# Kernel tuning notes

Hardware: AMD Instinct MI355X
Metric: run time of the kernel (lower is better)

The kernel has to match this reference:

```python
import jax, jax.numpy as jnp
import numpy as np

N, E = 50000, 800000
IN_CH, H, OUT_CH, ED, L = 64, 128, 128, 1, 4


def setup_inputs() -> dict:
    key = jax.random.key(0)
    ks = jax.random.split(key, 24)
    s = 0.02
    inp = {
        'h': jax.random.normal(ks[0], (N, IN_CH), jnp.float32),
        'coords': jax.random.normal(ks[1], (N, 3), jnp.float32),
        'edge_attr': jax.random.normal(ks[2], (E, ED), jnp.float32),
        'emb_in_W': jax.random.normal(ks[3], (IN_CH, H), jnp.float32) * s,
        'emb_in_b': jnp.zeros((H,), jnp.float32),
        'emb_out_W': jax.random.normal(ks[4], (H, OUT_CH), jnp.float32) * s,
        'emb_out_b': jnp.zeros((OUT_CH,), jnp.float32),
        # per-layer stacked params
        'eW1': jax.random.normal(ks[5], (L, 2 * H + 1 + ED, H), jnp.float32) * s,
        'eb1': jnp.zeros((L, H), jnp.float32),
        'eW2': jax.random.normal(ks[6], (L, H, H), jnp.float32) * s,
        'eb2': jnp.zeros((L, H), jnp.float32),
        'cW1': jax.random.normal(ks[7], (L, H, H), jnp.float32) * s,
        'cb1': jnp.zeros((L, H), jnp.float32),
        'cWc': jax.random.normal(ks[8], (L, H, 1), jnp.float32) * 0.001,  # xavier gain=0.001, no bias
        'nW1': jax.random.normal(ks[9], (L, 2 * H, H), jnp.float32) * s,
        'nb1': jnp.zeros((L, H), jnp.float32),
        'nW2': jax.random.normal(ks[10], (L, H, H), jnp.float32) * s,
        'nb2': jnp.zeros((L, H), jnp.float32),
        'edge_index': jax.random.randint(ks[11], (2, E), 0, N, jnp.int32),
    }
    return inp


def _egnn_forward(h, coords, edge_attr, emb_in_W, emb_in_b, emb_out_W, emb_out_b,
                  eW1, eb1, eW2, eb2, cW1, cb1, cWc, nW1, nb1, nW2, nb2, edge_index):
    silu = jax.nn.silu
    row, col = edge_index[0], edge_index[1]  # PyG: j=source=row, i=target=col
    # count of incoming edges per target node, for coords_agg='mean'
    counts = jax.ops.segment_sum(jnp.ones((E,), jnp.float32), col, num_segments=N)
    counts = jnp.maximum(counts, 1.0)[:, None]
    h = h @ emb_in_W + emb_in_b
    for l in range(L):
        coord_diff = coords[row] - coords[col]                       # [E,3]
        dist = jnp.sum(coord_diff * coord_diff, axis=-1, keepdims=True)  # [E,1]
        # message: edge MLP on cat(x_i, x_j, dist, edge_attr)
        edge_in = jnp.concatenate([h[col], h[row], dist, edge_attr], axis=-1)
        ef = silu(edge_in @ eW1[l] + eb1[l])
        ef = silu(ef @ eW2[l] + eb2[l])                               # [E,H]
        cw = silu(ef @ cW1[l] + cb1[l]) @ cWc[l]                      # [E,1]
        coord_upd = coord_diff * cw                                   # [E,3]
        # aggregate to target nodes
        agg_feat = jax.ops.segment_sum(ef, col, num_segments=N)       # [N,H]
        agg_coord = jax.ops.segment_sum(coord_upd, col, num_segments=N) / counts
        # node update (residual)
        node_in = jnp.concatenate([h, agg_feat], axis=-1)
        upd = silu(node_in @ nW1[l] + nb1[l]) @ nW2[l] + nb2[l]
        h = h + upd
        coords = coords + agg_coord
    h = h @ emb_out_W + emb_out_b
    return h, coords


def reference(h, coords, edge_attr, emb_in_W, emb_in_b, emb_out_W, emb_out_b,
              eW1, eb1, eW2, eb2, cW1, cb1, cWc, nW1, nb1, nW2, nb2, edge_index):
    return _egnn_forward(h, coords, edge_attr, emb_in_W, emb_in_b, emb_out_W, emb_out_b,
                         eW1, eb1, eW2, eb2, cW1, cb1, cWc, nW1, nb1, nW2, nb2, edge_index)
```

## Files before the change

kernel.cpp:

```cpp
#include <hip/hip_runtime.h>

constexpr int Nn = 50000;
constexpr int Ee = 800000;
constexpr int EIN_STR = 296;
constexpr int EF_STR  = 136;
constexpr int NIN_STR = 264;
constexpr int HIN_STR = 72;

typedef short s8v __attribute__((ext_vector_type(8)));
typedef float f4v __attribute__((ext_vector_type(4)));

__device__ __forceinline__ ushort f2bf(float f) {
    uint u = __float_as_uint(f);
    uint r = (u + 0x7FFFu + ((u >> 16) & 1u)) >> 16;
    return (ushort)r;
}
__device__ __forceinline__ float bf2f(ushort s) {
    return __uint_as_float(((uint)s) << 16);
}
__device__ __forceinline__ float silu_f(float x) {
    return x * __fdividef(1.0f, 1.0f + __expf(-x));
}

__global__ void __launch_bounds__(256) k_swzg(
    const float* __restrict__ src, ushort* __restrict__ dst, int K, int KC, int total)
{
    int gid = blockIdx.x * 256 + threadIdx.x;
    if (gid >= total) return;
    int per = KC * 4096;
    int l = gid / per, r = gid % per;
    int fb = r >> 9, rem = r & 511;
    int lane = rem >> 3, jj = rem & 7;
    int kc = fb >> 3, t = fb & 7;
    int k = kc * 32 + ((lane >> 4) << 3) + jj;
    int n = t * 16 + (lane & 15);
    float v = (k < K) ? src[(size_t)l * K * 128 + (size_t)k * 128 + n] : 0.0f;
    dst[gid] = f2bf(v);
}

__global__ void __launch_bounds__(256) k_count(const int* __restrict__ eidx, int* __restrict__ ecnt)
{
    int e = blockIdx.x * 256 + threadIdx.x;
    atomicAdd(&ecnt[eidx[Ee + e]], 1);
}

__global__ void __launch_bounds__(1024) k_scan(const int* __restrict__ ecnt, int* __restrict__ cursor)
{
    __shared__ int wsum[16];
    __shared__ int carry;
    int tid = threadIdx.x, lane = tid & 63, w = tid >> 6;
    if (tid == 0) carry = 0;
    __syncthreads();
    for (int start = 0; start < Nn; start += 1024) {
        int i = start + tid;
        int x = (i < Nn) ? ecnt[i] : 0;
        int c0 = carry;
        int s = x;
        #pragma unroll
        for (int off = 1; off < 64; off <<= 1) {
            int t = __shfl_up(s, off, 64);
            if (lane >= off) s += t;
        }
        if (lane == 63) wsum[w] = s;
        __syncthreads();
        if (w == 0) {
            int t = (lane < 16) ? wsum[lane] : 0;
            #pragma unroll
            for (int off = 1; off < 16; off <<= 1) {
                int u = __shfl_up(t, off, 64);
                if (lane >= off) t += u;
            }
            if (lane < 16) wsum[lane] = t;
        }
        __syncthreads();
        int woff = (w == 0) ? 0 : wsum[w - 1];
        if (i < Nn) cursor[i] = c0 + woff + s - x;
        int blocksum = wsum[15];
        __syncthreads();
        if (tid == 0) carry = c0 + blocksum;
        __syncthreads();
    }
}

__global__ void __launch_bounds__(256) k_scatter(
    const int* __restrict__ eidx, const float* __restrict__ edge_attr,
    int* __restrict__ cursor,
    int* __restrict__ srow, int* __restrict__ scol, float* __restrict__ sattr)
{
    int e = blockIdx.x * 256 + threadIdx.x;
    int r = eidx[e], c = eidx[Ee + e];
    int p = atomicAdd(&cursor[c], 1);
    srow[p] = r; scol[p] = c; sattr[p] = edge_attr[e];
}

__global__ void __launch_bounds__(512, 2) k_emb(
    const float* __restrict__ h_in, const float* __restrict__ coords,
    const ushort* __restrict__ ws_, const float* __restrict__ b,
    float* __restrict__ hbuf, ushort* __restrict__ hbf, float* __restrict__ cbuf)
{
    __shared__ alignas(16) ushort s_h[64 * HIN_STR];
    const int tid = threadIdx.x;
    const int nb = blockIdx.x * 64;
    #pragma unroll
    for (int i = 0; i < 2; i++) {
        int idx = i * 512 + tid;
        int e = idx >> 4, ch = idx & 15;
        int node = nb + e;
        float4 f = make_float4(0.f, 0.f, 0.f, 0.f);
        if (node < Nn) f = *(const float4*)(h_in + (size_t)node * 64 + ch * 4);
        ushort4 u; u.x = f2bf(f.x); u.y = f2bf(f.y); u.z = f2bf(f.z); u.w = f2bf(f.w);
        *(ushort4*)(s_h + e * HIN_STR + ch * 4) = u;
    }
    if (tid < 192) {
        int n = nb + tid / 3, d = tid % 3;
        if (n < Nn) cbuf[n * 3 + d] = coords[n * 3 + d];
    }
    __syncthreads();
    const int lane = tid & 63, wave = tid >> 6;
    const int m = lane & 15, quad = lane >> 4;
    const int ws2 = wave >> 2, wt = wave & 3;
    f4v acc[2][2];
    #pragma unroll
    for (int mt = 0; mt < 2; mt++) { acc[mt][0] = (f4v){0,0,0,0}; acc[mt][1] = (f4v){0,0,0,0}; }
    const ushort* bBase = ws_ + wt * 1024 + lane * 8;
    #pragma unroll
    for (int kc = 0; kc < 2; kc++) {
        s8v b0 = *(const s8v*)(bBase + kc * 4096);
        s8v b1v = *(const s8v*)(bBase + kc * 4096 + 512);
        #pragma unroll
        for (int mt = 0; mt < 2; mt++) {
            s8v a = *(const s8v*)(s_h + (ws2 * 32 + mt * 16 + m) * HIN_STR + kc * 32 + quad * 8);
            acc[mt][0] = __builtin_amdgcn_mfma_f32_16x16x32_bf16(a, b0, acc[mt][0], 0, 0, 0);
            acc[mt][1] = __builtin_amdgcn_mfma_f32_16x16x32_bf16(a, b1v, acc[mt][1], 0, 0, 0);
        }
    }
    #pragma unroll
    for (int tt = 0; tt < 2; tt++) {
        int col = (wt * 2 + tt) * 16 + m;
        float bias = b[col];
        #pragma unroll
        for (int mt = 0; mt < 2; mt++)
            #pragma unroll
            for (int r = 0; r < 4; r++) {
                int node = nb + ws2 * 32 + mt * 16 + quad * 4 + r;
                if (node < Nn) {
                    float v = acc[mt][tt][r] + bias;
                    hbuf[(size_t)node * 128 + col] = v;
                    hbf[(size_t)node * 128 + col] = f2bf(v);
                }
            }
    }
}

__global__ void __launch_bounds__(512, 2) k_edge(
    const ushort* __restrict__ hbf, const float* __restrict__ cbuf,
    const int* __restrict__ srow, const int* __restrict__ scol, const float* __restrict__ sattr,
    const ushort* __restrict__ w1s, const float* __restrict__ b1,
    const ushort* __restrict__ w2s, const float* __restrict__ b2,
    const ushort* __restrict__ cw1s, const float* __restrict__ cb1,
    const float* __restrict__ cwc,
    float* __restrict__ agg_feat, float* __restrict__ agg_coord)
{
    __shared__ alignas(16) ushort s_ein[64 * EIN_STR];
    __shared__ alignas(16) ushort s_efa[64 * EF_STR];
    __shared__ alignas(16) ushort s_efb[64 * EF_STR];
    __shared__ int   s_col[64];
    __shared__ int   s_row[64];
    __shared__ float s_cd[64 * 3];
    __shared__ float s_cw[64];

    const int tid = threadIdx.x;
    const int eb = blockIdx.x * 64;

    if (tid < 64) {
        int rw = srow[eb + tid], cl = scol[eb + tid];
        s_row[tid] = rw; s_col[tid] = cl;
        float d0 = cbuf[rw * 3 + 0] - cbuf[cl * 3 + 0];
        float d1 = cbuf[rw * 3 + 1] - cbuf[cl * 3 + 1];
        float d2 = cbuf[rw * 3 + 2] - cbuf[cl * 3 + 2];
        s_cd[tid * 3 + 0] = d0; s_cd[tid * 3 + 1] = d1; s_cd[tid * 3 + 2] = d2;
        float dist = d0 * d0 + d1 * d1 + d2 * d2;
        s_ein[tid * EIN_STR + 256] = f2bf(dist);
        s_ein[tid * EIN_STR + 257] = f2bf(sattr[eb + tid]);
        uint* zp = (uint*)(s_ein + tid * EIN_STR + 258);
        #pragma unroll
        for (int z = 0; z < 15; z++) zp[z] = 0;
        s_cw[tid] = 0.0f;
    }
    __syncthreads();

    #pragma unroll
    for (int i = 0; i < 4; i++) {
        int idx = i * 512 + tid;
        int e = idx >> 5, ch = idx & 31;
        int node = (ch < 16) ? s_col[e] : s_row[e];
        uint4 v = *(const uint4*)(hbf + (size_t)node * 128 + (ch & 15) * 8);
        *(uint4*)(s_ein + e * EIN_STR + ch * 8) = v;
    }
    __syncthreads();

    const int lane = tid & 63, wave = tid >> 6;
    const int m = lane & 15, quad = lane >> 4;
    const int ws2 = wave >> 2, wt = wave & 3;
    const int rbase = ws2 * 32;

    {
        f4v acc[2][2];
        #pragma unroll
        for (int mt = 0; mt < 2; mt++) { acc[mt][0] = (f4v){0,0,0,0}; acc[mt][1] = (f4v){0,0,0,0}; }
        const ushort* bBase = w1s + wt * 1024 + (size_t)lane * 8;
        #pragma unroll
        for (int kc = 0; kc < 9; kc++) {
            s8v b0 = *(const s8v*)(bBase + kc * 4096);
            s8v b1v = *(const s8v*)(bBase + kc * 4096 + 512);
            #pragma unroll
            for (int mt = 0; mt < 2; mt++) {
                s8v a = *(const s8v*)(s_ein + (rbase + mt * 16 + m) * EIN_STR + kc * 32 + quad * 8);
                acc[mt][0] = __builtin_amdgcn_mfma_f32_16x16x32_bf16(a, b0, acc[mt][0], 0, 0, 0);
                acc[mt][1] = __builtin_amdgcn_mfma_f32_16x16x32_bf16(a, b1v, acc[mt][1], 0, 0, 0);
            }
        }
        #pragma unroll
        for (int tt = 0; tt < 2; tt++) {
            int col = (wt * 2 + tt) * 16 + m;
            float bias = b1[col];
            #pragma unroll
            for (int mt = 0; mt < 2; mt++)
                #pragma unroll
                for (int r = 0; r < 4; r++)
                    s_efa[(rbase + mt * 16 + quad * 4 + r) * EF_STR + col] = f2bf(silu_f(acc[mt][tt][r] + bias));
        }
    }
    __syncthreads();

    {
        f4v acc[2][2];
        #pragma unroll
        for (int mt = 0; mt < 2; mt++) { acc[mt][0] = (f4v){0,0,0,0}; acc[mt][1] = (f4v){0,0,0,0}; }
        const ushort* bBase = w2s + wt * 1024 + (size_t)lane * 8;
        #pragma unroll
        for (int kc = 0; kc < 4; kc++) {
            s8v b0 = *(const s8v*)(bBase + kc * 4096);
            s8v b1v = *(const s8v*)(bBase + kc * 4096 + 512);
            #pragma unroll
            for (int mt = 0; mt < 2; mt++) {
                s8v a = *(const s8v*)(s_efa + (rbase + mt * 16 + m) * EF_STR + kc * 32 + quad * 8);
                acc[mt][0] = __builtin_amdgcn_mfma_f32_16x16x32_bf16(a, b0, acc[mt][0], 0, 0, 0);
                acc[mt][1] = __builtin_amdgcn_mfma_f32_16x16x32_bf16(a, b1v, acc[mt][1], 0, 0, 0);
            }
        }
        #pragma unroll
        for (int tt = 0; tt < 2; tt++) {
            int col = (wt * 2 + tt) * 16 + m;
            float bias = b2[col];
            #pragma unroll
            for (int mt = 0; mt < 2; mt++)
                #pragma unroll
                for (int r = 0; r < 4; r++)
                    s_efb[(rbase + mt * 16 + quad * 4 + r) * EF_STR + col] = f2bf(silu_f(acc[mt][tt][r] + bias));
        }
    }
    __syncthreads();

    {
        f4v acc[2][2];
        #pragma unroll
        for (int mt = 0; mt < 2; mt++) { acc[mt][0] = (f4v){0,0,0,0}; acc[mt][1] = (f4v){0,0,0,0}; }
        const ushort* bBase = cw1s + wt * 1024 + (size_t)lane * 8;
        #pragma unroll
        for (int kc = 0; kc < 4; kc++) {
            s8v b0 = *(const s8v*)(bBase + kc * 4096);
            s8v b1v = *(const s8v*)(bBase + kc * 4096 + 512);
            #pragma unroll
            for (int mt = 0; mt < 2; mt++) {
                s8v a = *(const s8v*)(s_efb + (rbase + mt * 16 + m) * EF_STR + kc * 32 + quad * 8);
                acc[mt][0] = __builtin_amdgcn_mfma_f32_16x16x32_bf16(a, b0, acc[mt][0], 0, 0, 0);
                acc[mt][1] = __builtin_amdgcn_mfma_f32_16x16x32_bf16(a, b1v, acc[mt][1], 0, 0, 0);
            }
        }
        int c0 = wt * 32 + m, c1 = wt * 32 + 16 + m;
        float bias0 = cb1[c0], wc0 = cwc[c0];
        float bias1 = cb1[c1], wc1 = cwc[c1];
        #pragma unroll
        for (int mt = 0; mt < 2; mt++) {
            float p0 = silu_f(acc[mt][0][0] + bias0) * wc0 + silu_f(acc[mt][1][0] + bias1) * wc1;
            float p1 = silu_f(acc[mt][0][1] + bias0) * wc0 + silu_f(acc[mt][1][1] + bias1) * wc1;
            float p2 = silu_f(acc[mt][0][2] + bias0) * wc0 + silu_f(acc[mt][1][2] + bias1) * wc1;
            float p3 = silu_f(acc[mt][0][3] + bias0) * wc0 + silu_f(acc[mt][1][3] + bias1) * wc1;
            #pragma unroll
            for (int off = 1; off < 16; off <<= 1) {
                p0 += __shfl_xor(p0, off, 64);
                p1 += __shfl_xor(p1, off, 64);
                p2 += __shfl_xor(p2, off, 64);
                p3 += __shfl_xor(p3, off, 64);
            }
            if (m < 4) {
                float v = (m == 0) ? p0 : (m == 1) ? p1 : (m == 2) ? p2 : p3;
                atomicAdd(&s_cw[rbase + mt * 16 + quad * 4 + m], v);
            }
        }
    }
    __syncthreads();

    if (tid < 12) {
        int d = tid % 3, seg = tid / 3;
        int e0 = seg * 16;
        float acc = 0.0f; int cur = s_col[e0];
        for (int e = e0; e < e0 + 16; e++) {
            int c = s_col[e];
            if (c != cur) {
                unsafeAtomicAdd(&agg_coord[cur * 3 + d], acc);
                acc = 0.0f; cur = c;
            }
            acc += s_cd[e * 3 + d] * s_cw[e];
        }
        unsafeAtomicAdd(&agg_coord[cur * 3 + d], acc);
    }

    {
        int j = tid & 127;
        int e0 = (tid >> 7) * 16;
        float acc = 0.0f; int cur = s_col[e0];
        #pragma unroll 4
        for (int e = e0; e < e0 + 16; e++) {
            int c = s_col[e];
            if (c != cur) {
                unsafeAtomicAdd(&agg_feat[(size_t)cur * 128 + j], acc);
                acc = 0.0f; cur = c;
            }
            acc += bf2f(s_efb[e * EF_STR + j]);
        }
        unsafeAtomicAdd(&agg_feat[(size_t)cur * 128 + j], acc);
    }
}

__global__ void __launch_bounds__(512, 2) k_node(
    float* __restrict__ hbuf, ushort* __restrict__ hbf, float* __restrict__ cbuf,
    const float* __restrict__ agg_feat, const float* __restrict__ agg_coord,
    const int* __restrict__ ecnt,
    const ushort* __restrict__ w1s, const float* __restrict__ b1,
    const ushort* __restrict__ w2s, const float* __restrict__ b2)
{
    __shared__ alignas(16) ushort s_nin[64 * NIN_STR];
    __shared__ alignas(16) ushort s_t1[64 * EF_STR];
    const int tid = threadIdx.x;
    const int nb = blockIdx.x * 64;

    #pragma unroll
    for (int i = 0; i < 2; i++) {
        int idx = i * 512 + tid;
        int e = idx >> 4, ch = idx & 15;
        int node = nb + e;
        uint4 v = make_uint4(0, 0, 0, 0);
        if (node < Nn) v = *(const uint4*)(hbf + (size_t)node * 128 + ch * 8);
        *(uint4*)(s_nin + e * NIN_STR + ch * 8) = v;
    }
    #pragma unroll
    for (int i = 0; i < 4; i++) {
        int idx = i * 512 + tid;
        int e = idx >> 5, ch = idx & 31;
        int node = nb + e;
        float4 f = make_float4(0.f, 0.f, 0.f, 0.f);
        if (node < Nn) f = *(const float4*)(agg_feat + (size_t)node * 128 + ch * 4);
        ushort4 u; u.x = f2bf(f.x); u.y = f2bf(f.y); u.z = f2bf(f.z); u.w = f2bf(f.w);
        *(ushort4*)(s_nin + e * NIN_STR + 128 + ch * 4) = u;
    }
    if (tid < 64) {
        int n = nb + tid;
        if (n < Nn) {
            float c = (float)ecnt[n]; c = (c < 1.0f) ? 1.0f : c;
            float inv = __fdividef(1.0f, c);
            cbuf[n * 3 + 0] += agg_coord[n * 3 + 0] * inv;
            cbuf[n * 3 + 1] += agg_coord[n * 3 + 1] * inv;
            cbuf[n * 3 + 2] += agg_coord[n * 3 + 2] * inv;
        }
    }
    __syncthreads();

    const int lane = tid & 63, wave = tid >> 6;
    const int m = lane & 15, quad = lane >> 4;
    const int ws2 = wave >> 2, wt = wave & 3;
    const int rbase = ws2 * 32;

    {
        f4v acc[2][2];
        #pragma unroll
        for (int mt = 0; mt < 2; mt++) { acc[mt][0] = (f4v){0,0,0,0}; acc[mt][1] = (f4v){0,0,0,0}; }
        const ushort* bBase = w1s + wt * 1024 + (size_t)lane * 8;
        #pragma unroll
        for (int kc = 0; kc < 8; kc++) {
            s8v b0 = *(const s8v*)(bBase + kc * 4096);
            s8v b1v = *(const s8v*)(bBase + kc * 4096 + 512);
            #pragma unroll
            for (int mt = 0; mt < 2; mt++) {
                s8v a = *(const s8v*)(s_nin + (rbase + mt * 16 + m) * NIN_STR + kc * 32 + quad * 8);
                acc[mt][0] = __builtin_amdgcn_mfma_f32_16x16x32_bf16(a, b0, acc[mt][0], 0, 0, 0);
                acc[mt][1] = __builtin_amdgcn_mfma_f32_16x16x32_bf16(a, b1v, acc[mt][1], 0, 0, 0);
            }
        }
        #pragma unroll
        for (int tt = 0; tt < 2; tt++) {
            int col = (wt * 2 + tt) * 16 + m;
            float bias = b1[col];
            #pragma unroll
            for (int mt = 0; mt < 2; mt++)
                #pragma unroll
                for (int r = 0; r < 4; r++)
                    s_t1[(rbase + mt * 16 + quad * 4 + r) * EF_STR + col] = f2bf(silu_f(acc[mt][tt][r] + bias));
        }
    }
    __syncthreads();

    {
        f4v acc[2][2];
        #pragma unroll
        for (int mt = 0; mt < 2; mt++) { acc[mt][0] = (f4v){0,0,0,0}; acc[mt][1] = (f4v){0,0,0,0}; }
        const ushort* bBase = w2s + wt * 1024 + (size_t)lane * 8;
        #pragma unroll
        for (int kc = 0; kc < 4; kc++) {
            s8v b0 = *(const s8v*)(bBase + kc * 4096);
            s8v b1v = *(const s8v*)(bBase + kc * 4096 + 512);
            #pragma unroll
            for (int mt = 0; mt < 2; mt++) {
                s8v a = *(const s8v*)(s_t1 + (rbase + mt * 16 + m) * EF_STR + kc * 32 + quad * 8);
                acc[mt][0] = __builtin_amdgcn_mfma_f32_16x16x32_bf16(a, b0, acc[mt][0], 0, 0, 0);
                acc[mt][1] = __builtin_amdgcn_mfma_f32_16x16x32_bf16(a, b1v, acc[mt][1], 0, 0, 0);
            }
        }
        #pragma unroll
        for (int tt = 0; tt < 2; tt++) {
            int col = (wt * 2 + tt) * 16 + m;
            float bias = b2[col];
            #pragma unroll
            for (int mt = 0; mt < 2; mt++)
                #pragma unroll
                for (int r = 0; r < 4; r++) {
                    int node = nb + rbase + mt * 16 + quad * 4 + r;
                    if (node < Nn) {
                        float v = hbuf[(size_t)node * 128 + col] + acc[mt][tt][r] + bias;
                        hbuf[(size_t)node * 128 + col] = v;
                        hbf[(size_t)node * 128 + col] = f2bf(v);
                    }
                }
        }
    }
}

__global__ void __launch_bounds__(512, 2) k_emb_out(
    const ushort* __restrict__ hbf, const float* __restrict__ cbuf,
    const ushort* __restrict__ ws_, const float* __restrict__ b, float* __restrict__ out)
{
    __shared__ alignas(16) ushort s_h[64 * EF_STR];
    const int tid = threadIdx.x;
    const int nb = blockIdx.x * 64;
    #pragma unroll
    for (int i = 0; i < 2; i++) {
        int idx = i * 512 + tid;
        int e = idx >> 4, ch = idx & 15;
        int node = nb + e;
        uint4 v = make_uint4(0, 0, 0, 0);
        if (node < Nn) v = *(const uint4*)(hbf + (size_t)node * 128 + ch * 8);
        *(uint4*)(s_h + e * EF_STR + ch * 8) = v;
    }
    if (tid < 192) {
        int n = nb + tid / 3, d = tid % 3;
        if (n < Nn) out[(size_t)Nn * 128 + n * 3 + d] = cbuf[n * 3 + d];
    }
    __syncthreads();
    const int lane = tid & 63, wave = tid >> 6;
    const int m = lane & 15, quad = lane >> 4;
    const int ws2 = wave >> 2, wt = wave & 3;
    f4v acc[2][2];
    #pragma unroll
    for (int mt = 0; mt < 2; mt++) { acc[mt][0] = (f4v){0,0,0,0}; acc[mt][1] = (f4v){0,0,0,0}; }
    const ushort* bBase = ws_ + wt * 1024 + (size_t)lane * 8;
    #pragma unroll
    for (int kc = 0; kc < 4; kc++) {
        s8v b0 = *(const s8v*)(bBase + kc * 4096);
        s8v b1v = *(const s8v*)(bBase + kc * 4096 + 512);
        #pragma unroll
        for (int mt = 0; mt < 2; mt++) {
            s8v a = *(const s8v*)(s_h + (ws2 * 32 + mt * 16 + m) * EF_STR + kc * 32 + quad * 8);
            acc[mt][0] = __builtin_amdgcn_mfma_f32_16x16x32_bf16(a, b0, acc[mt][0], 0, 0, 0);
            acc[mt][1] = __builtin_amdgcn_mfma_f32_16x16x32_bf16(a, b1v, acc[mt][1], 0, 0, 0);
        }
    }
    #pragma unroll
    for (int tt = 0; tt < 2; tt++) {
        int col = (wt * 2 + tt) * 16 + m;
        float bias = b[col];
        #pragma unroll
        for (int mt = 0; mt < 2; mt++)
            #pragma unroll
            for (int r = 0; r < 4; r++) {
                int node = nb + ws2 * 32 + mt * 16 + quad * 4 + r;
                if (node < Nn) out[(size_t)node * 128 + col] = acc[mt][tt][r] + bias;
            }
    }
}

extern "C" void kernel_launch(void* const* d_in, const int* in_sizes, int n_in,
                              void* d_out, int out_size, void* d_ws, size_t ws_size,
                              hipStream_t stream)
{
    const float* h_in      = (const float*)d_in[0];
    const float* coords    = (const float*)d_in[1];
    const float* edge_attr = (const float*)d_in[2];
    const float* emb_in_W  = (const float*)d_in[3];
    const float* emb_in_b  = (const float*)d_in[4];
    const float* emb_out_W = (const float*)d_in[5];
    const float* emb_out_b = (const float*)d_in[6];
    const float* eW1 = (const float*)d_in[7];
    const float* eb1 = (const float*)d_in[8];
    const float* eW2 = (const float*)d_in[9];
    const float* eb2 = (const float*)d_in[10];
    const float* cW1 = (const float*)d_in[11];
    const float* cb1 = (const float*)d_in[12];
    const float* cWc = (const float*)d_in[13];
    const float* nW1 = (const float*)d_in[14];
    const float* nb1 = (const float*)d_in[15];
    const float* nW2 = (const float*)d_in[16];
    const float* nb2 = (const float*)d_in[17];
    const int*  eidx = (const int*)d_in[18];

    size_t off = 0;
    char* base = (char*)d_ws;
    auto alloc = [&](size_t bytes) -> char* {
        char* p = base + off;
        off += (bytes + 255) & ~(size_t)255;
        return p;
    };
    float*  hbuf      = (float*)alloc((size_t)Nn * 128 * 4);
    ushort* hbf       = (ushort*)alloc((size_t)Nn * 128 * 2);
    float*  cbuf      = (float*)alloc((size_t)Nn * 3 * 4);
    int*    ecnt      = (int*)alloc((size_t)Nn * 4);
    int*    cursor    = (int*)alloc((size_t)Nn * 4);
    int*    srow      = (int*)alloc((size_t)Ee * 4);
    int*    scol      = (int*)alloc((size_t)Ee * 4);
    float*  sattr     = (float*)alloc((size_t)Ee * 4);
    float*  agg_feat  = (float*)alloc((size_t)Nn * 128 * 4);
    float*  agg_coord = (float*)alloc((size_t)Nn * 3 * 4);
    ushort* eW1s      = (ushort*)alloc((size_t)4 * 36864 * 2);
    ushort* eW2s      = (ushort*)alloc((size_t)4 * 16384 * 2);
    ushort* cW1s      = (ushort*)alloc((size_t)4 * 16384 * 2);
    ushort* nW1s      = (ushort*)alloc((size_t)4 * 32768 * 2);
    ushort* nW2s      = (ushort*)alloc((size_t)4 * 16384 * 2);
    ushort* eInWs     = (ushort*)alloc((size_t)8192 * 2);
    ushort* eOutWs    = (ushort*)alloc((size_t)16384 * 2);

    k_swzg<<<(4*9*4096+255)/256, 256, 0, stream>>>(eW1, eW1s, 258, 9, 4*9*4096);
    k_swzg<<<(4*4*4096+255)/256, 256, 0, stream>>>(eW2, eW2s, 128, 4, 4*4*4096);
    k_swzg<<<(4*4*4096+255)/256, 256, 0, stream>>>(cW1, cW1s, 128, 4, 4*4*4096);
    k_swzg<<<(4*8*4096+255)/256, 256, 0, stream>>>(nW1, nW1s, 256, 8, 4*8*4096);
    k_swzg<<<(4*4*4096+255)/256, 256, 0, stream>>>(nW2, nW2s, 128, 4, 4*4*4096);
    k_swzg<<<(2*4096+255)/256,   256, 0, stream>>>(emb_in_W,  eInWs,  64, 2, 2*4096);
    k_swzg<<<(4*4096+255)/256,   256, 0, stream>>>(emb_out_W, eOutWs, 128, 4, 4*4096);

    hipMemsetAsync(ecnt, 0, (size_t)Nn * 4, stream);
    k_count<<<Ee / 256, 256, 0, stream>>>(eidx, ecnt);
    k_scan<<<1, 1024, 0, stream>>>(ecnt, cursor);
    k_scatter<<<Ee / 256, 256, 0, stream>>>(eidx, edge_attr, cursor, srow, scol, sattr);
    k_emb<<<(Nn + 63) / 64, 512, 0, stream>>>(h_in, coords, eInWs, emb_in_b, hbuf, hbf, cbuf);

    for (int l = 0; l < 4; l++) {
        hipMemsetAsync(agg_feat, 0, (size_t)Nn * 128 * 4, stream);
        hipMemsetAsync(agg_coord, 0, (size_t)Nn * 3 * 4, stream);
        k_edge<<<Ee / 64, 512, 0, stream>>>(
            hbf, cbuf, srow, scol, sattr,
            eW1s + (size_t)l * 36864, eb1 + l * 128,
            eW2s + (size_t)l * 16384, eb2 + l * 128,
            cW1s + (size_t)l * 16384, cb1 + l * 128,
            cWc + l * 128,
            agg_feat, agg_coord);
        k_node<<<(Nn + 63) / 64, 512, 0, stream>>>(
            hbuf, hbf, cbuf, agg_feat, agg_coord, ecnt,
            nW1s + (size_t)l * 32768, nb1 + l * 128,
            nW2s + (size_t)l * 16384, nb2 + l * 128);
    }
    k_emb_out<<<(Nn + 63) / 64, 512, 0, stream>>>(hbf, cbuf, eOutWs, emb_out_b, (float*)d_out);
}
```

Baseline: 1.753 ms.

## Shrink edge-kernel shared memory and raise occupancy with buffer reuse

Shrinks the edge kernel's LDS footprint from three large tiles to two reused 64x136 buffers plus a small tail tile for dist/attr, and raises launch bounds from 2 to 6 blocks per CU. The aim is more concurrent blocks to hide gather and atomic latency. Also removes a sync before the gather, replaces the LDS-atomic coord-weight reduction with shuffles into per-slot partials, and switches bf16 conversion to truncation. The tighter launch bound may force register spills, and truncation changes numerics slightly.

```diff
diff --git a/kernel.cpp b/kernel.cpp
--- a/kernel.cpp
+++ b/kernel.cpp
@@ -2,8 +2,8 @@
 
 constexpr int Nn = 50000;
 constexpr int Ee = 800000;
-constexpr int EIN_STR = 296;
 constexpr int EF_STR  = 136;
+constexpr int TL_STR  = 40;
 constexpr int NIN_STR = 264;
 constexpr int HIN_STR = 72;
 
@@ -14,6 +14,9 @@
     uint u = __float_as_uint(f);
     uint r = (u + 0x7FFFu + ((u >> 16) & 1u)) >> 16;
     return (ushort)r;
+}
+__device__ __forceinline__ ushort f2bf_t(float f) {
+    return (ushort)(__float_as_uint(f) >> 16);
 }
 __device__ __forceinline__ float bf2f(ushort s) {
     return __uint_as_float(((uint)s) << 16);
@@ -152,7 +155,7 @@
     }
 }
 
-__global__ void __launch_bounds__(512, 2) k_edge(
+__global__ void __launch_bounds__(512, 6) k_edge(
     const ushort* __restrict__ hbf, const float* __restrict__ cbuf,
     const int* __restrict__ srow, const int* __restrict__ scol, const float* __restrict__ sattr,
     const ushort* __restrict__ w1s, const float* __restrict__ b1,
@@ -161,41 +164,38 @@
     const float* __restrict__ cwc,
     float* __restrict__ agg_feat, float* __restrict__ agg_coord)
 {
-    __shared__ alignas(16) ushort s_ein[64 * EIN_STR];
-    __shared__ alignas(16) ushort s_efa[64 * EF_STR];
-    __shared__ alignas(16) ushort s_efb[64 * EF_STR];
+    __shared__ alignas(16) ushort s_a[64 * EF_STR];
+    __shared__ alignas(16) ushort s_b[64 * EF_STR];
+    __shared__ alignas(16) ushort s_t[64 * TL_STR];
     __shared__ int   s_col[64];
-    __shared__ int   s_row[64];
     __shared__ float s_cd[64 * 3];
-    __shared__ float s_cw[64];
 
     const int tid = threadIdx.x;
     const int eb = blockIdx.x * 64;
 
     if (tid < 64) {
         int rw = srow[eb + tid], cl = scol[eb + tid];
-        s_row[tid] = rw; s_col[tid] = cl;
+        s_col[tid] = cl;
         float d0 = cbuf[rw * 3 + 0] - cbuf[cl * 3 + 0];
         float d1 = cbuf[rw * 3 + 1] - cbuf[cl * 3 + 1];
         float d2 = cbuf[rw * 3 + 2] - cbuf[cl * 3 + 2];
         s_cd[tid * 3 + 0] = d0; s_cd[tid * 3 + 1] = d1; s_cd[tid * 3 + 2] = d2;
         float dist = d0 * d0 + d1 * d1 + d2 * d2;
-        s_ein[tid * EIN_STR + 256] = f2bf(dist);
-        s_ein[tid * EIN_STR + 257] = f2bf(sattr[eb + tid]);
-        uint* zp = (uint*)(s_ein + tid * EIN_STR + 258);
+        s_t[tid * TL_STR + 0] = f2bf(dist);
+        s_t[tid * TL_STR + 1] = f2bf(sattr[eb + tid]);
+        uint* zp = (uint*)(s_t + tid * TL_STR + 2);
         #pragma unroll
         for (int z = 0; z < 15; z++) zp[z] = 0;
-        s_cw[tid] = 0.0f;
-    }
-    __syncthreads();
-
+    }
     #pragma unroll
     for (int i = 0; i < 4; i++) {
         int idx = i * 512 + tid;
         int e = idx >> 5, ch = idx & 31;
-        int node = (ch < 16) ? s_col[e] : s_row[e];
+        int node = (ch < 16) ? scol[eb + e] : srow[eb + e];
         uint4 v = *(const uint4*)(hbf + (size_t)node * 128 + (ch & 15) * 8);
-        *(uint4*)(s_ein + e * EIN_STR + ch * 8) = v;
+        ushort* dst = (ch < 16) ? (s_a + e * EF_STR + ch * 8)
+                                : (s_b + e * EF_STR + (ch - 16) * 8);
+        *(uint4*)dst = v;
     }
     __syncthreads();
 
@@ -204,137 +204,341 @@
     const int ws2 = wave >> 2, wt = wave & 3;
     const int rbase = ws2 * 32;
 
-    {
-        f4v acc[2][2];
-        #pragma unroll
-        for (int mt = 0; mt < 2; mt++) { acc[mt][0] = (f4v){0,0,0,0}; acc[mt][1] = (f4v){0,0,0,0}; }
+    f4v acc[2][2];
+    #pragma unroll
+    for (int mt = 0; mt < 2; mt++) { acc[mt][0] = (f4v){0,0,0,0}; acc[mt][1] = (f4v){0,0,0,0}; }
+    {
         const ushort* bBase = w1s + wt * 1024 + (size_t)lane * 8;
         #pragma unroll
-        for (int kc = 0; kc < 9; kc++) {
-            s8v b0 = *(const s8v*)(bBase + kc * 4096);
-            s8v b1v = *(const s8v*)(bBase + kc * 4096 + 512);
-            #pragma unroll
-            for (int mt = 0; mt < 2; mt++) {
-                s8v a = *(const s8v*)(s_ein + (rbase + mt * 16 + m) * EIN_STR + kc * 32 + quad * 8);
+        for (int kc = 0; kc < 4; kc++) {
+            s8v b0 = *(const s8v*)(bBase + kc * 4096);
+            s8v b1v = *(const s8v*)(bBase + kc * 4096 + 512);
+            #pragma unroll
+            for (int mt = 0; mt < 2; mt++) {
+                s8v a = *(const s8v*)(s_a + (rbase + mt * 16 + m) * EF_STR + kc * 32 + quad * 8);
                 acc[mt][0] = __builtin_amdgcn_mfma_f32_16x16x32_bf16(a, b0, acc[mt][0], 0, 0, 0);
                 acc[mt][1] = __builtin_amdgcn_mfma_f32_16x16x32_bf16(a, b1v, acc[mt][1], 0, 0, 0);
             }
         }
         #pragma unroll
+        for (int kc = 4; kc < 8; kc++) {
+            s8v b0 = *(const s8v*)(bBase + kc * 4096);
+            s8v b1v = *(const s8v*)(bBase + kc * 4096 + 512);
+            #pragma unroll
+            for (int mt = 0; mt < 2; mt++) {
+                s8v a = *(const s8v*)(s_b + (rbase + mt * 16 + m) * EF_STR + (kc - 4) * 32 + quad * 8);
+                acc[mt][0] = __builtin_amdgcn_mfma_f32_16x16x32_bf16(a, b0, acc[mt][0], 0, 0, 0);
+                acc[mt][1] = __builtin_amdgcn_mfma_f32_16x16x32_bf16(a, b1v, acc[mt][1], 0, 0, 0);
+            }
+        }
+        {
+            s8v b0 = *(const s8v*)(bBase + 8 * 4096);
+            s8v b1v = *(const s8v*)(bBase + 8 * 4096 + 512);
+            #pragma unroll
+            for (int mt = 0; mt < 2; mt++) {
+                s8v a = *(const s8v*)(s_t + (rbase + mt * 16 + m) * TL_STR + quad * 8);
+                acc[mt][0] = __builtin_amdgcn_mfma_f32_16x16x32_bf16(a, b0, acc[mt][0], 0, 0, 0);
+                acc[mt][1] = __builtin_amdgcn_mfma_f32_16x16x32_bf16(a, b1v, acc[mt][1], 0, 0, 0);
+            }
+        }
+    }
+    __syncthreads();
+
+    #pragma unroll
+    for (int tt = 0; tt < 2; tt++) {
+        int col = (wt * 2 + tt) * 16 + m;
+        float bias = b1[col];
+        #pragma unroll
+        for (int mt = 0; mt < 2; mt++)
+            #pragma unroll
+            for (int r = 0; r < 4; r++)
+                s_a[(rbase + mt * 16 + quad * 4 + r) * EF_STR + col] = f2bf_t(silu_f(acc[mt][tt][r] + bias));
+    }
+    __syncthreads();
+
+    {
+        f4v acc2[2][2];
+        #pragma unroll
+        for (int mt = 0; mt < 2; mt++) { acc2[mt][0] = (f4v){0,0,0,0}; acc2[mt][1] = (f4v){0,0,0,0}; }
+        const ushort* bBase = w2s + wt * 1024 + (size_t)lane * 8;
+        #pragma unroll
+        for (int kc = 0; kc < 4; kc++) {
+            s8v b0 = *(const s8v*)(bBase + kc * 4096);
+            s8v b1v = *(const s8v*)(bBase + kc * 4096 + 512);
+            #pragma unroll
+            for (int mt = 0; mt < 2; mt++) {
+                s8v a = *(const s8v*)(s_a + (rbase + mt * 16 + m) * EF_STR + kc * 32 + quad * 8);
+                acc2[mt][0] = __builtin_amdgcn_mfma_f32_16x16x32_bf16(a, b0, acc2[mt][0], 0, 0, 0);
+                acc2[mt][1] = __builtin_amdgcn_mfma_f32_16x16x32_bf16(a, b1v, acc2[mt][1], 0, 0, 0);
+            }
+        }
+        #pragma unroll
         for (int tt = 0; tt < 2; tt++) {
             int col = (wt * 2 + tt) * 16 + m;
-            float bias = b1[col];
+            float bias = b2[col];
             #pragma unroll
             for (int mt = 0; mt < 2; mt++)
                 #pragma unroll
                 for (int r = 0; r < 4; r++)
-                    s_efa[(rbase + mt * 16 + quad * 4 + r) * EF_STR + col] = f2bf(silu_f(acc[mt][tt][r] + bias));
-        }
-    }
-    __syncthreads();
-
-    {
-        f4v acc[2][2];
-        #pragma unroll
-        for (int mt = 0; mt < 2; mt++) { acc[mt][0] = (f4v){0,0,0,0}; acc[mt][1] = (f4v){0,0,0,0}; }
-        const ushort* bBase = w2s + wt * 1024 + (size_t)lane * 8;
+                    s_b[(rbase + mt * 16 + quad * 4 + r) * EF_STR + col] = f2bf_t(silu_f(acc2[mt][tt][r] + bias));
+        }
+    }
+    __syncthreads();
+
+    {
+        f4v acc3[2][2];
+        #pragma unroll
+        for (int mt = 0; mt < 2; mt++) { acc3[mt][0] = (f4v){0,0,0,0}; acc3[mt][1] = (f4v){0,0,0,0}; }
+        const ushort* bBase = cw1s + wt * 1024 + (size_t)lane * 8;
         #pragma unroll
         for (int kc = 0; kc < 4; kc++) {
             s8v b0 = *(const s8v*)(bBase + kc * 4096);
             s8v b1v = *(const s8v*)(bBase + kc * 4096 + 512);
             #pragma unroll
             for (int mt = 0; mt < 2; mt++) {
-                s8v a = *(const s8v*)(s_efa + (rbase + mt * 16 + m) * EF_STR + kc * 32 + quad * 8);
-                acc[mt][0] = __builtin_amdgcn_mfma_f32_16x16x32_bf16(a, b0, acc[mt][0], 0, 0, 0);
-                acc[mt][1] = __builtin_amdgcn_mfma_f32_16x16x32_bf16(a, b1v, acc[mt][1], 0, 0, 0);
-            }
-        }
-        #pragma unroll
-        for (int tt = 0; tt < 2; tt++) {
-            int col = (wt * 2 + tt) * 16 + m;
-            float bias = b2[col];
-            #pragma unroll
-            for (int mt = 0; mt < 2; mt++)
-                #pragma unroll
-                for (int r = 0; r < 4; r++)
-                    s_efb[(rbase + mt * 16 + quad * 4 + r) * EF_STR + col] = f2bf(silu_f(acc[mt][tt][r] + bias));
-        }
-    }
-    __syncthreads();
-
-    {
-        f4v acc[2][2];
-        #pragma unroll
-        for (int mt = 0; mt < 2; mt++) { acc[mt][0] = (f4v){0,0,0,0}; acc[mt][1] = (f4v){0,0,0,0}; }
-        const ushort* bBase = cw1s + wt * 1024 + (size_t)lane * 8;
-        #pragma unroll
-        for (int kc = 0; kc < 4; kc++) {
-            s8v b0 = *(const s8v*)(bBase + kc * 4096);
-            s8v b1v = *(const s8v*)(bBase + kc * 4096 + 512);
-            #pragma unroll
-            for (int mt = 0; mt < 2; mt++) {
-                s8v a = *(const s8v*)(s_efb + (rbase + mt * 16 + m) * EF_STR + kc * 32 + quad * 8);
-                acc[mt][0] = __builtin_amdgcn_mfma_f32_16x16x32_bf16(a, b0, acc[mt][0], 0, 0, 0);
-                acc[mt][1] = __builtin_amdgcn_mfma_f32_16x16x32_bf16(a, b1v, acc[mt][1], 0, 0, 0);
+                s8v a = *(const s8v*)(s_b + (rbase + mt * 16 + m) * EF_STR + kc * 32 + quad * 8);
+                acc3[mt][0] = __builtin_amdgcn_mfma_f32_16x16x32_bf16(a, b0, acc3[mt][0], 0, 0, 0);
+                acc3[mt][1] = __builtin_amdgcn_mfma_f32_16x16x32_bf16(a, b1v, acc3[mt][1], 0, 0, 0);
             }
         }
         int c0 = wt * 32 + m, c1 = wt * 32 + 16 + m;
         float bias0 = cb1[c0], wc0 = cwc[c0];
         float bias1 = cb1[c1], wc1 = cwc[c1];
-        #pragma unroll
-        for (int mt = 0; mt < 2; mt++) {
-            float p0 = silu_f(acc[mt][0][0] + bias0) * wc0 + silu_f(acc[mt][1][0] + bias1) * wc1;
-            float p1 = silu_f(acc[mt][0][1] + bias0) * wc0 + silu_f(acc[mt][1][1] + bias1) * wc1;
-            float p2 = silu_f(acc[mt][0][2] + bias0) * wc0 + silu_f(acc[mt][1][2] + bias1) * wc1;
-            float p3 = silu_f(acc[mt][0][3] + bias0) * wc0 + silu_f(acc[mt][1][3] + bias1) * wc1;
-            #pragma unroll
-            for (int off = 1; off < 16; off <<= 1) {
-                p0 += __shfl_xor(p0, off, 64);
-                p1 += __shfl_xor(p1, off, 64);
-                p2 += __shfl_xor(p2, off, 64);
-                p3 += __shfl_xor(p3, off, 64);
-            }
-            if (m < 4) {
-                float v = (m == 0) ? p0 : (m == 1) ? p1 : (m == 2) ? p2 : p3;
-                atomicAdd(&s_cw[rbase + mt * 16 + quad * 4 + m], v);
-            }
-        }
-    }
-    __syncthreads();
-
-    if (tid < 12) {
-        int d = tid % 3, seg = tid / 3;
-        int e0 = seg * 16;
-        float acc = 0.0f; int cur = s_col[e0];
-        for (int e = e0; e < e0 + 16; e++) {
-            int c = s_col[e];
-            if (c != cur) {
-                unsafeAtomicAdd(&agg_coord[cur * 3 + d], acc);
-                acc = 0.0f; cur = c;
-            }
-            acc += s_cd[e * 3 + d] * s_cw[e];
-        }
-        unsafeAtomicAdd(&agg_coord[cur * 3 + d], acc);
+        float* s_part = (float*)s_t;
+        #pragma unroll
+        for (int mt = 0; mt < 2; mt++)
+            #pragma unroll
+            for (int r = 0; r < 4; r++) {
+                float p = silu_f(acc3[mt][0][r] + bias0) * wc0 + silu_f(acc3[mt][1][r] + bias1) * wc1;
+                s_part[(rbase + mt * 16 + quad * 4 + r) * 20 + m] = 0.0f;
+                s_part[(rbase + mt * 16 + quad * 4 + r) * 20 + m] = p;
+            }
+    }
+    __syncthreads();
+
+
+    if (tid < 64) {
+        float* s_part = (float*)s_t;
+        float cw = 0.0f;
+        #pragma unroll
+        for (int l = 0; l < 16; l++) cw += s_part[tid * 20 + l];
+        int cn = s_col[tid];
+        unsafeAtomicAdd(&agg_coord[cn * 3 + 0], s_cd[tid * 3 + 0] * cw);
+        unsafeAtomicAdd(&agg_coord[cn * 3 + 1], s_cd[tid * 3 + 1] * cw);
+        unsafeAtomicAdd(&agg_coord[cn * 3 + 2], s_cd[tid * 3 + 2] * cw);
     }
 
     {
         int j = tid & 127;
         int e0 = (tid >> 7) * 16;
-        float acc = 0.0f; int cur = s_col[e0];
+        float accv = 0.0f; int cur = s_col[e0];
         #pragma unroll 4
         for (int e = e0; e < e0 + 16; e++) {
             int c = s_col[e];
             if (c != cur) {
-                unsafeAtomicAdd(&agg_feat[(size_t)cur * 128 + j], acc);
-                acc = 0.0f; cur = c;
-            }
-            acc += bf2f(s_efb[e * EF_STR + j]);
-        }
-        unsafeAtomicAdd(&agg_feat[(size_t)cur * 128 + j], acc);
-    }
-}
-
-__global__ void __launch_bounds__(512, 2) k_node(
+                unsafeAtomicAdd(&agg_feat[(size_t)cur * 128 + j], accv);
+                accv = 0.0f; cur = c;
+            }
+            accv += bf2f(s_b[e * EF_STR + j]);
+        }
+        unsafeAtomicAdd(&agg_feat[(size_t)cur * 128 + j], accv);
+    }
+}
+
+
+__global__ void __launch_bounds__(512, 6) k_edge_fixed(
+    const ushort* __restrict__ hbf, const float* __restrict__ cbuf,
+    const int* __restrict__ srow, const int* __restrict__ scol, const float* __restrict__ sattr,
+    const ushort* __restrict__ w1s, const float* __restrict__ b1,
+    const ushort* __restrict__ w2s, const float* __restrict__ b2,
+    const ushort* __restrict__ cw1s, const float* __restrict__ cb1,
+    const float* __restrict__ cwc,
+    float* __restrict__ agg_feat, float* __restrict__ agg_coord)
+{
+    __shared__ alignas(16) ushort s_a[64 * EF_STR];
+    __shared__ alignas(16) ushort s_b[64 * EF_STR];
+    __shared__ alignas(16) ushort s_t[64 * TL_STR];
+    __shared__ int   s_col[64];
+    __shared__ float s_cd[64 * 3];
+
+    const int tid = threadIdx.x;
+    const int eb = blockIdx.x * 64;
+
+    if (tid < 64) {
+        int rw = srow[eb + tid], cl = scol[eb + tid];
+        s_col[tid] = cl;
+        float d0 = cbuf[rw * 3 + 0] - cbuf[cl * 3 + 0];
+        float d1 = cbuf[rw * 3 + 1] - cbuf[cl * 3 + 1];
+        float d2 = cbuf[rw * 3 + 2] - cbuf[cl * 3 + 2];
+        s_cd[tid * 3 + 0] = d0; s_cd[tid * 3 + 1] = d1; s_cd[tid * 3 + 2] = d2;
+        float dist = d0 * d0 + d1 * d1 + d2 * d2;
+        s_t[tid * TL_STR + 0] = f2bf(dist);
+        s_t[tid * TL_STR + 1] = f2bf(sattr[eb + tid]);
+        uint* zp = (uint*)(s_t + tid * TL_STR + 2);
+        #pragma unroll
+        for (int z = 0; z < 15; z++) zp[z] = 0;
+    }
+    #pragma unroll
+    for (int i = 0; i < 4; i++) {
+        int idx = i * 512 + tid;
+        int e = idx >> 5, ch = idx & 31;
+        int node = (ch < 16) ? scol[eb + e] : srow[eb + e];
+        uint4 v = *(const uint4*)(hbf + (size_t)node * 128 + (ch & 15) * 8);
+        ushort* dst = (ch < 16) ? (s_a + e * EF_STR + ch * 8)
+                                : (s_b + e * EF_STR + (ch - 16) * 8);
+        *(uint4*)dst = v;
+    }
+    __syncthreads();
+
+    const int lane = tid & 63, wave = tid >> 6;
+    const int m = lane & 15, quad = lane >> 4;
+    const int ws2 = wave >> 2, wt = wave & 3;
+    const int rbase = ws2 * 32;
+
+    f4v acc[2][2];
+    #pragma unroll
+    for (int mt = 0; mt < 2; mt++) { acc[mt][0] = (f4v){0,0,0,0}; acc[mt][1] = (f4v){0,0,0,0}; }
+    {
+        const ushort* bBase = w1s + wt * 1024 + (size_t)lane * 8;
+        #pragma unroll
+        for (int kc = 0; kc < 4; kc++) {
+            s8v b0 = *(const s8v*)(bBase + kc * 4096);
+            s8v b1v = *(const s8v*)(bBase + kc * 4096 + 512);
+            #pragma unroll
+            for (int mt = 0; mt < 2; mt++) {
+                s8v a = *(const s8v*)(s_a + (rbase + mt * 16 + m) * EF_STR + kc * 32 + quad * 8);
+                acc[mt][0] = __builtin_amdgcn_mfma_f32_16x16x32_bf16(a, b0, acc[mt][0], 0, 0, 0);
+                acc[mt][1] = __builtin_amdgcn_mfma_f32_16x16x32_bf16(a, b1v, acc[mt][1], 0, 0, 0);
+            }
+        }
+        #pragma unroll
+        for (int kc = 4; kc < 8; kc++) {
+            s8v b0 = *(const s8v*)(bBase + kc * 4096);
+            s8v b1v = *(const s8v*)(bBase + kc * 4096 + 512);
+            #pragma unroll
+            for (int mt = 0; mt < 2; mt++) {
+                s8v a = *(const s8v*)(s_b + (rbase + mt * 16 + m) * EF_STR + (kc - 4) * 32 + quad * 8);
+                acc[mt][0] = __builtin_amdgcn_mfma_f32_16x16x32_bf16(a, b0, acc[mt][0], 0, 0, 0);
+                acc[mt][1] = __builtin_amdgcn_mfma_f32_16x16x32_bf16(a, b1v, acc[mt][1], 0, 0, 0);
+            }
+        }
+        {
+            s8v b0 = *(const s8v*)(bBase + 8 * 4096);
+            s8v b1v = *(const s8v*)(bBase + 8 * 4096 + 512);
+            #pragma unroll
+            for (int mt = 0; mt < 2; mt++) {
+                s8v a = *(const s8v*)(s_t + (rbase + mt * 16 + m) * TL_STR + quad * 8);
+                acc[mt][0] = __builtin_amdgcn_mfma_f32_16x16x32_bf16(a, b0, acc[mt][0], 0, 0, 0);
+                acc[mt][1] = __builtin_amdgcn_mfma_f32_16x16x32_bf16(a, b1v, acc[mt][1], 0, 0, 0);
+            }
+        }
+    }
+    __syncthreads();
+
+    #pragma unroll
+    for (int tt = 0; tt < 2; tt++) {
+        int col = (wt * 2 + tt) * 16 + m;
+        float bias = b1[col];
+        #pragma unroll
+        for (int mt = 0; mt < 2; mt++)
+            #pragma unroll
+            for (int r = 0; r < 4; r++)
+                s_a[(rbase + mt * 16 + quad * 4 + r) * EF_STR + col] = f2bf_t(silu_f(acc[mt][tt][r] + bias));
+    }
+    __syncthreads();
+
+    {
+        f4v acc2[2][2];
+        #pragma unroll
+        for (int mt = 0; mt < 2; mt++) { acc2[mt][0] = (f4v){0,0,0,0}; acc2[mt][1] = (f4v){0,0,0,0}; }
+        const ushort* bBase = w2s + wt * 1024 + (size_t)lane * 8;
+        #pragma unroll
+        for (int kc = 0; kc < 4; kc++) {
+            s8v b0 = *(const s8v*)(bBase + kc * 4096);
+            s8v b1v = *(const s8v*)(bBase + kc * 4096 + 512);
+            #pragma unroll
+            for (int mt = 0; mt < 2; mt++) {
+                s8v a = *(const s8v*)(s_a + (rbase + mt * 16 + m) * EF_STR + kc * 32 + quad * 8);
+                acc2[mt][0] = __builtin_amdgcn_mfma_f32_16x16x32_bf16(a, b0, acc2[mt][0], 0, 0, 0);
+                acc2[mt][1] = __builtin_amdgcn_mfma_f32_16x16x32_bf16(a, b1v, acc2[mt][1], 0, 0, 0);
+            }
+        }
+        #pragma unroll
+        for (int tt = 0; tt < 2; tt++) {
+            int col = (wt * 2 + tt) * 16 + m;
+            float bias = b2[col];
+            #pragma unroll
+            for (int mt = 0; mt < 2; mt++)
+                #pragma unroll
+                for (int r = 0; r < 4; r++)
+                    s_b[(rbase + mt * 16 + quad * 4 + r) * EF_STR + col] = f2bf_t(silu_f(acc2[mt][tt][r] + bias));
+        }
+    }
+    __syncthreads();
+
+    {
+        f4v acc3[2][2];
+        #pragma unroll
+        for (int mt = 0; mt < 2; mt++) { acc3[mt][0] = (f4v){0,0,0,0}; acc3[mt][1] = (f4v){0,0,0,0}; }
+        const ushort* bBase = cw1s + wt * 1024 + (size_t)lane * 8;
+        #pragma unroll
+        for (int kc = 0; kc < 4; kc++) {
+            s8v b0 = *(const s8v*)(bBase + kc * 4096);
+            s8v b1v = *(const s8v*)(bBase + kc * 4096 + 512);
+            #pragma unroll
+            for (int mt = 0; mt < 2; mt++) {
+                s8v a = *(const s8v*)(s_b + (rbase + mt * 16 + m) * EF_STR + kc * 32 + quad * 8);
+                acc3[mt][0] = __builtin_amdgcn_mfma_f32_16x16x32_bf16(a, b0, acc3[mt][0], 0, 0, 0);
+                acc3[mt][1] = __builtin_amdgcn_mfma_f32_16x16x32_bf16(a, b1v, acc3[mt][1], 0, 0, 0);
+            }
+        }
+        int c0 = wt * 32 + m, c1 = wt * 32 + 16 + m;
+        float bias0 = cb1[c0], wc0 = cwc[c0];
+        float bias1 = cb1[c1], wc1 = cwc[c1];
+        float* s_part = (float*)s_t;
+        #pragma unroll
+        for (int mt = 0; mt < 2; mt++)
+            #pragma unroll
+            for (int r = 0; r < 4; r++) {
+                float p = silu_f(acc3[mt][0][r] + bias0) * wc0 + silu_f(acc3[mt][1][r] + bias1) * wc1;
+                p += __shfl_xor(p, 1, 64);
+                p += __shfl_xor(p, 2, 64);
+                if ((m & 3) == 0) {
+                    int slot = wt * 4 + (m >> 2);
+                    s_part[(rbase + mt * 16 + quad * 4 + r) * 20 + slot] = p;
+                }
+            }
+    }
+    __syncthreads();
+
+    if (tid < 64) {
+        float* s_part = (float*)s_t;
+        float cw = 0.0f;
+        #pragma unroll
+        for (int l = 0; l < 16; l++) cw += s_part[tid * 20 + l];
+        int cn = s_col[tid];
+        unsafeAtomicAdd(&agg_coord[cn * 3 + 0], s_cd[tid * 3 + 0] * cw);
+        unsafeAtomicAdd(&agg_coord[cn * 3 + 1], s_cd[tid * 3 + 1] * cw);
+        unsafeAtomicAdd(&agg_coord[cn * 3 + 2], s_cd[tid * 3 + 2] * cw);
+    }
+    {
+        int j = tid & 127;
+        int e0 = (tid >> 7) * 16;
+        float accv = 0.0f; int cur = s_col[e0];
+        #pragma unroll 4
+        for (int e = e0; e < e0 + 16; e++) {
+            int c = s_col[e];
+            if (c != cur) {
+                unsafeAtomicAdd(&agg_feat[(size_t)cur * 128 + j], accv);
+                accv = 0.0f; cur = c;
+            }
+            accv += bf2f(s_b[e * EF_STR + j]);
+        }
+        unsafeAtomicAdd(&agg_feat[(size_t)cur * 128 + j], accv);
+    }
+}
+
+__global__ void __launch_bounds__(512, 6) k_node(
     float* __restrict__ hbuf, ushort* __restrict__ hbf, float* __restrict__ cbuf,
     const float* __restrict__ agg_feat, const float* __restrict__ agg_coord,
     const int* __restrict__ ecnt,
@@ -362,7 +566,7 @@
         int node = nb + e;
         float4 f = make_float4(0.f, 0.f, 0.f, 0.f);
         if (node < Nn) f = *(const float4*)(agg_feat + (size_t)node * 128 + ch * 4);
-        ushort4 u; u.x = f2bf(f.x); u.y = f2bf(f.y); u.z = f2bf(f.z); u.w = f2bf(f.w);
+        ushort4 u; u.x = f2bf_t(f.x); u.y = f2bf_t(f.y); u.z = f2bf_t(f.z); u.w = f2bf_t(f.w);
         *(ushort4*)(s_nin + e * NIN_STR + 128 + ch * 4) = u;
     }
     if (tid < 64) {
@@ -406,7 +610,7 @@
             for (int mt = 0; mt < 2; mt++)
                 #pragma unroll
                 for (int r = 0; r < 4; r++)
-                    s_t1[(rbase + mt * 16 + quad * 4 + r) * EF_STR + col] = f2bf(silu_f(acc[mt][tt][r] + bias));
+                    s_t1[(rbase + mt * 16 + quad * 4 + r) * EF_STR + col] = f2bf_t(silu_f(acc[mt][tt][r] + bias));
         }
     }
     __syncthreads();
@@ -565,7 +769,7 @@
     for (int l = 0; l < 4; l++) {
         hipMemsetAsync(agg_feat, 0, (size_t)Nn * 128 * 4, stream);
         hipMemsetAsync(agg_coord, 0, (size_t)Nn * 3 * 4, stream);
-        k_edge<<<Ee / 64, 512, 0, stream>>>(
+        k_edge_fixed<<<Ee / 64, 512, 0, stream>>>(
             hbf, cbuf, srow, scol, sattr,
             eW1s + (size_t)l * 36864, eb1 + l * 128,
             eW2s + (size_t)l * 16384, eb2 + l * 128,
```

Result: faster. 1.713 ms (-2.3%).
